# Performance work log

Measured on AMD Instinct MI355X. Metric: run time of the kernel, lower is better.

The kernel has to match this reference:

```python
import jax, jax.numpy as jnp
import numpy as np

D = 2048
N = 4096          # context length
H = N + 1         # Z columns (context + query)
LMBD = 0.9


def _decay_mask(h, n, lmbd, dtype=jnp.float32):
    # Closed form of the serial recurrence: M[r, c] = lmbd**(r-c) for c <= r < n, c < n; else 0.
    r = jnp.arange(h)
    diff = r[:, None] - r[None, :]
    valid = (diff >= 0) & (r[:, None] < n) & (r[None, :] < n)
    pow_ = jnp.asarray(lmbd, dtype) ** jnp.maximum(diff, 0).astype(dtype)
    return jnp.where(valid, pow_, jnp.zeros((), dtype))


def setup_inputs() -> dict:
    key = jax.random.key(0)
    kz, kp, kq = jax.random.split(key, 3)
    dim = 2 * D + 1
    Z = jax.random.normal(kz, (dim, H), dtype=jnp.float32)
    # params scaled like a typical init to keep the 5-GEMM chain numerically tame
    P = jax.random.normal(kp, (dim, dim), dtype=jnp.float32) * 0.02
    Q = jax.random.normal(kq, (dim, dim), dtype=jnp.float32) * 0.02
    return {"Z": Z, "P": P, "Q": Q}


def reference(Z, P, Q):
    h = Z.shape[1]
    M = _decay_mask(h, N, LMBD, Z.dtype)          # (h, h)
    left = (P @ Z) @ M                            # (2d+1, h)
    right = Z.T @ (Q @ Z)                         # (h, h)
    return Z + (left @ right) / N
```

## Files before the change

kernel.cpp:

```cpp
#include <hip/hip_runtime.h>


typedef __attribute__((ext_vector_type(8))) short short8;
typedef __attribute__((ext_vector_type(4))) float f32x4;
typedef __attribute__((ext_vector_type(4))) unsigned short u16x4;

#define NPAD 4352
#define NV   4097
#define NCTX 4096
#define NT   65
#define NT4  64

__device__ __forceinline__ float b2f(unsigned short u) {
  return __uint_as_float(((unsigned)u) << 16);
}
__device__ __forceinline__ unsigned short f2b(float f) {
  unsigned b = __float_as_uint(f);
  return (unsigned short)((b + 0x7FFFu + ((b >> 16) & 1u)) >> 16);
}
__device__ __forceinline__ void gload16(const void* g, void* l) {
  __builtin_amdgcn_global_load_lds(
      (const __attribute__((address_space(1))) unsigned int*)g,
      (__attribute__((address_space(3))) unsigned int*)l, 16, 0, 0);
}
__device__ __forceinline__ float wave_sum(float v) {
#pragma unroll
  for (int m = 1; m < 64; m <<= 1) v += __shfl_xor(v, m);
  return v;
}

__global__ __launch_bounds__(256) void cast_pad(const float* __restrict__ in,
                                                unsigned short* __restrict__ out) {
  int idx = blockIdx.x * 256 + threadIdx.x;
  int r = idx / 1088;
  int c4 = (idx - r * 1088) * 4;
  u16x4 o = {0, 0, 0, 0};
  if (r < NV) {
    const float* p = in + (size_t)r * NV + c4;
#pragma unroll
    for (int j = 0; j < 4; ++j) {
      float v = (c4 + j < NV) ? p[j] : 0.f;
      o[j] = f2b(v);
    }
  }
  *(u16x4*)&out[(size_t)r * NPAD + c4] = o;
}

__global__ __launch_bounds__(256) void transpose_cast(const float* __restrict__ in,
                                                      unsigned short* __restrict__ out) {
  __shared__ float tile[32][33];
  int x = threadIdx.x & 31;
  int y = threadIdx.x >> 5;
  int bx = blockIdx.x, by = blockIdx.y;
  int ic = bx * 32 + x;
#pragma unroll
  for (int j = 0; j < 4; ++j) {
    int ir = by * 32 + y + j * 8;
    float v = (ir < NV && ic < NV) ? in[(size_t)ir * NV + ic] : 0.f;
    tile[y + j * 8][x] = v;
  }
  __syncthreads();
  int orow = bx * 32;
  int ocol = by * 32 + x;
#pragma unroll
  for (int j = 0; j < 4; ++j) {
    out[(size_t)(orow + y + j * 8) * NPAD + ocol] = f2b(tile[x][y + j * 8]);
  }
}

__global__ __launch_bounds__(256) void decay_scan(const unsigned short* __restrict__ PZ,
                                                  unsigned short* __restrict__ L) {
  const int wid = (blockIdx.x << 2) | ((int)threadIdx.x >> 6);
  if (wid >= NV * 65) return;
  const int lane = threadIdx.x & 63;
  const int row = wid / 65;
  const int cj = wid - row * 65;
  const int c0 = cj * 64;

  const float l2l = -0.15200309344504995f;
  const float pl = exp2f((float)lane * l2l);
  const float plc = exp2f((float)(64 - lane) * l2l);

  const unsigned short* prow = PZ + (size_t)row * NPAD;
  float x[5];
#pragma unroll
  for (int d = 0; d < 5; ++d) {
    int c = c0 + d * 64 + lane;
    x[d] = (c < NCTX) ? b2f(prow[c]) : 0.f;
  }
  float s = x[0];
  const float pw[6] = {0.9f, 0.81f, 0.6561f, 0.43046721f,
                       0.18530201888518410f, 0.03433683820292512f};
#pragma unroll
  for (int i = 0; i < 6; ++i) {
    int tt = 1 << i;
    float o = __shfl_down(s, tt);
    s += (lane + tt < 64) ? pw[i] * o : 0.f;
  }
  const float cw[4] = {1.f, 1.1790184577738583e-3f, 1.3900845237714557e-6f,
                       1.6389541800e-9f};
  float carry = 0.f;
#pragma unroll
  for (int d = 1; d <= 4; ++d) {
    float v = x[d] * pl;
#pragma unroll
    for (int i = 0; i < 6; ++i) v += __shfl_xor(v, 1 << i);
    carry += cw[d - 1] * v;
  }
  float left = s + plc * carry;
  L[(size_t)row * NPAD + c0 + lane] = f2b(left);
}

template <int MODE>
__global__ __launch_bounds__(512, 2) void gemm256(
    const unsigned short* __restrict__ A0, const unsigned short* __restrict__ Bt0,
    unsigned short* __restrict__ C0,
    const unsigned short* __restrict__ A1, const unsigned short* __restrict__ Bt1,
    unsigned short* __restrict__ C1,
    float* __restrict__ Cf, const float* __restrict__ Zin) {
  __shared__ __align__(16) unsigned short Asm[2][256 * 64];
  __shared__ __align__(16) unsigned short Bsm[2][256 * 64];

  const int tid = threadIdx.x;
  const int lane = tid & 63;
  const int w = tid >> 6;
  const int wr = w >> 2, wc = w & 3;
  const int q = lane >> 4, r16 = lane & 15;

  const int NFULL = (MODE == 0) ? 512 : 256;
  const int cpx = NFULL >> 3;
  int orig = blockIdx.x;
  int wg = (orig & 7) * cpx + (orig >> 3);

  const unsigned short* Am;
  const unsigned short* Btm;
  unsigned short* Co;
  if (MODE == 0) {
    int batch = wg >> 8;
    Am = batch ? A1 : A0;
    Btm = batch ? Bt1 : Bt0;
    Co = batch ? C1 : C0;
    wg &= 255;
  } else {
    Am = A0; Btm = Bt0; Co = C0;
  }
  const int by = wg >> 4, bx = wg & 15;
  const int brow = by * 256, bcol = bx * 256;
  const int KE = (MODE == 2) ? NT4 : NT;

  auto stageA = [&](int ktile, int mq, int bb) {
#pragma unroll
    for (int it = 0; it < 2; ++it) {
      int sub = w * 16 + it * 8;
      int row0 = mq * 64 + sub + (sub & 64);
      int row = row0 + (lane >> 3);
      int win = (lane & 7) ^ (row & 7);
      gload16(Am + (size_t)(brow + row) * NPAD + ktile * 64 + win * 8,
              &Asm[bb][row0 * 64]);
    }
  };
  auto stageB = [&](int ktile, int nq, int bb) {
#pragma unroll
    for (int it = 0; it < 2; ++it) {
      int sub = w * 16 + it * 8;
      int row0 = ((sub >> 5) << 6) + nq * 32 + (sub & 31);
      int row = row0 + (lane >> 3);
      int win = (lane & 7) ^ (row & 7);
      gload16(Btm + (size_t)(bcol + row) * NPAD + ktile * 64 + win * 8,
              &Bsm[bb][row0 * 64]);
    }
  };

  short8 a[4][2], b0r[2][2], b1r[2][2];
  auto rdA = [&](int mq, int bb) {
#pragma unroll
    for (int m = 0; m < 4; ++m) {
      int row = wr * 128 + mq * 64 + m * 16 + r16;
#pragma unroll
      for (int kk = 0; kk < 2; ++kk) {
        int win = (q + kk * 4) ^ (r16 & 7);
        a[m][kk] = *(const short8*)&Asm[bb][row * 64 + win * 8];
      }
    }
  };
  auto rdB = [&](short8 (&b)[2][2], int nq, int bb) {
#pragma unroll
    for (int n = 0; n < 2; ++n) {
      int row = wc * 64 + nq * 32 + n * 16 + r16;
#pragma unroll
      for (int kk = 0; kk < 2; ++kk) {
        int win = (q + kk * 4) ^ (r16 & 7);
        b[n][kk] = *(const short8*)&Bsm[bb][row * 64 + win * 8];
      }
    }
  };

  f32x4 acc[8][4] = {};

  auto mma2 = [&](int mq) {
    __builtin_amdgcn_s_setprio(1);
#pragma unroll
    for (int kk = 0; kk < 2; ++kk)
#pragma unroll
      for (int m = 0; m < 4; ++m) {
#pragma unroll
        for (int n = 0; n < 2; ++n)
          acc[mq * 4 + m][n] = __builtin_amdgcn_mfma_f32_16x16x32_bf16(
              a[m][kk], b0r[n][kk], acc[mq * 4 + m][n], 0, 0, 0);
#pragma unroll
        for (int n = 0; n < 2; ++n)
          acc[mq * 4 + m][2 + n] = __builtin_amdgcn_mfma_f32_16x16x32_bf16(
              a[m][kk], b1r[n][kk], acc[mq * 4 + m][2 + n], 0, 0, 0);
      }
    __builtin_amdgcn_s_setprio(0);
  };

  stageA(0, 0, 0); stageB(0, 0, 0); stageA(0, 1, 0); stageB(0, 1, 0);
  stageA(1, 0, 1); stageB(1, 0, 1);
  asm volatile("s_waitcnt vmcnt(4)" ::: "memory");
  __builtin_amdgcn_s_barrier();

  for (int kt = 0; kt < KE; ++kt) {
    const int bb = kt & 1;
    rdA(0, bb);
    rdB(b0r, 0, bb);
    rdB(b1r, 1, bb);
    if (kt + 1 < KE) { stageA(kt + 1, 1, bb ^ 1); stageB(kt + 1, 1, bb ^ 1); }
    __builtin_amdgcn_s_barrier();
    mma2(0);
    __builtin_amdgcn_s_barrier();
    rdA(1, bb);
    if (kt + 2 < KE) { stageA(kt + 2, 0, bb); stageB(kt + 2, 0, bb); }
    if (kt < KE - 2) { asm volatile("s_waitcnt vmcnt(4)" ::: "memory"); }
    else             { asm volatile("s_waitcnt vmcnt(0)" ::: "memory"); }
    __builtin_amdgcn_s_barrier();
    mma2(1);
    __builtin_amdgcn_s_barrier();
  }

#pragma unroll
  for (int m = 0; m < 8; ++m) {
    const int row = brow + wr * 128 + m * 16 + q * 4;
#pragma unroll
    for (int n = 0; n < 4; ++n) {
      const int col = bcol + wc * 64 + n * 16 + r16;
#pragma unroll
      for (int v = 0; v < 4; ++v) {
        float val = acc[m][n][v];
        if (MODE == 2) {
          size_t o = (size_t)(row + v) * NV + col;
          Cf[o] = Zin[o] + val * (1.0f / 4096.0f);
        } else {
          Co[(size_t)(row + v) * NPAD + col] = f2b(val);
        }
      }
    }
  }
}

__global__ __launch_bounds__(256) void border1(
    const unsigned short* __restrict__ Pb, const unsigned short* __restrict__ Qb,
    const unsigned short* __restrict__ Zt,
    unsigned short* __restrict__ PZ, unsigned short* __restrict__ QZt) {
  const int wid = blockIdx.x * 4 + ((int)threadIdx.x >> 6);
  const int lane = threadIdx.x & 63;
  if (wid < 4096) {
    const int t = wid;
    const unsigned short* z = Zt + (size_t)t * NPAD;
    const unsigned short* p = Pb + (size_t)4096 * NPAD;
    const unsigned short* qq = Qb + (size_t)4096 * NPAD;
    float ap = 0.f, aq = 0.f;
    for (int k = lane * 8; k < 4104; k += 512) {
      short8 zv = *(const short8*)&z[k];
      short8 pv = *(const short8*)&p[k];
      short8 qv = *(const short8*)&qq[k];
#pragma unroll
      for (int j = 0; j < 8; ++j) {
        float zf = b2f((unsigned short)zv[j]);
        ap += zf * b2f((unsigned short)pv[j]);
        aq += zf * b2f((unsigned short)qv[j]);
      }
    }
    ap = wave_sum(ap);
    aq = wave_sum(aq);
    if (lane == 0) PZ[(size_t)4096 * NPAD + t] = f2b(ap);
    QZt[(size_t)t * NPAD + 4096 + lane] = (lane == 0) ? f2b(aq) : (unsigned short)0;
  } else {
    const int j = wid - 4096;
    if (j >= 4160) return;
    const unsigned short* qr = Qb + (size_t)j * NPAD;
    const unsigned short* zr = Zt + (size_t)4096 * NPAD;
    float a = 0.f;
    for (int k = lane * 8; k < 4104; k += 512) {
      short8 qv = *(const short8*)&qr[k];
      short8 zv = *(const short8*)&zr[k];
#pragma unroll
      for (int jj = 0; jj < 8; ++jj)
        a += b2f((unsigned short)qv[jj]) * b2f((unsigned short)zv[jj]);
    }
    a = wave_sum(a);
    if (lane == 0) QZt[(size_t)4096 * NPAD + j] = f2b(a);
  }
}

__global__ __launch_bounds__(256) void border2(const unsigned short* __restrict__ QZt,
                                               const unsigned short* __restrict__ Zt,
                                               unsigned short* __restrict__ RT) {
  const int t = blockIdx.x * 4 + ((int)threadIdx.x >> 6);
  const int lane = threadIdx.x & 63;
  const unsigned short* a = QZt + (size_t)4096 * NPAD;
  const unsigned short* z = Zt + (size_t)t * NPAD;
  float s = 0.f;
  for (int k = lane * 8; k < 4104; k += 512) {
    short8 av = *(const short8*)&a[k];
    short8 zv = *(const short8*)&z[k];
#pragma unroll
    for (int j = 0; j < 8; ++j)
      s += b2f((unsigned short)av[j]) * b2f((unsigned short)zv[j]);
  }
  s = wave_sum(s);
  if (lane == 0) RT[(size_t)4096 * NPAD + t] = f2b(s);
}

__global__ __launch_bounds__(256) void border3(const unsigned short* __restrict__ L,
                                               const unsigned short* __restrict__ RT,
                                               const float* __restrict__ Z,
                                               float* __restrict__ out) {
  const int wid = blockIdx.x * 4 + ((int)threadIdx.x >> 6);
  const int lane = threadIdx.x & 63;
  const unsigned short *lr, *rr;
  size_t o;
  if (wid < 4097) {
    lr = L + (size_t)4096 * NPAD;
    rr = RT + (size_t)wid * NPAD;
    o = (size_t)4096 * NV + wid;
  } else {
    const int r = wid - 4097;
    if (r >= 4096) return;
    lr = L + (size_t)r * NPAD;
    rr = RT + (size_t)4096 * NPAD;
    o = (size_t)r * NV + 4096;
  }
  float s = 0.f;
#pragma unroll 2
  for (int i = 0; i < 8; ++i) {
    int k = lane * 8 + i * 512;
    short8 lv = *(const short8*)&lr[k];
    short8 rv = *(const short8*)&rr[k];
#pragma unroll
    for (int j = 0; j < 8; ++j)
      s += b2f((unsigned short)lv[j]) * b2f((unsigned short)rv[j]);
  }
  s = wave_sum(s);
  if (lane == 0) out[o] = Z[o] + s * (1.0f / 4096.0f);
}

extern "C" void kernel_launch(void* const* d_in, const int* in_sizes, int n_in,
                              void* d_out, int out_size, void* d_ws, size_t ws_size,
                              hipStream_t stream) {
  (void)in_sizes; (void)n_in; (void)out_size; (void)ws_size;
  const float* Z = (const float*)d_in[0];
  const float* P = (const float*)d_in[1];
  const float* Q = (const float*)d_in[2];
  float* out = (float*)d_out;

  const size_t SZ = (size_t)NPAD * NPAD;
  unsigned short* b0 = (unsigned short*)d_ws;
  unsigned short* b1 = b0 + SZ;
  unsigned short* b2 = b1 + SZ;
  unsigned short* b3 = b2 + SZ;
  unsigned short* dox = (unsigned short*)d_out;

  dim3 blk(256), blk5(512);
  dim3 gt(136, 136);

  cast_pad<<<18496, blk, 0, stream>>>(P, b0);
  cast_pad<<<18496, blk, 0, stream>>>(Q, b3);
  transpose_cast<<<gt, blk, 0, stream>>>(Z, b1);
  gemm256<0><<<512, blk5, 0, stream>>>(b0, b1, b2, b1, b3, dox, nullptr, nullptr);
  border1<<<2064, blk, 0, stream>>>(b0, b3, b1, b2, dox);
  decay_scan<<<66577, blk, 0, stream>>>(b2, b0);
  gemm256<1><<<256, blk5, 0, stream>>>(dox, b1, b2, nullptr, nullptr, nullptr,
                                       nullptr, nullptr);
  border2<<<1024, blk, 0, stream>>>(dox, b1, b2);
  gemm256<2><<<256, blk5, 0, stream>>>(b0, b2, nullptr, nullptr, nullptr, nullptr,
                                       out, Z);
  border3<<<2049, blk, 0, stream>>>(b0, b2, Z, out);
}
```

Baseline: 666.8 us.

## Drop redundant GEMM barriers, widen decay scan per wave, merge cast kernels

Removes two of the four workgroup barriers per k-iteration in the main GEMM loop, on the reasoning that the remaining barriers already order LDS reuse between the staged buffers. The decay scan now has each wave handle four 64-column chunks and reuse the butterfly-reduced sums across overlapping carry windows, which cuts the number of waves and redundant shuffles. The two P/Q cast launches are merged into one grid. Risks: fewer barriers could expose LDS races. The scan no longer writes the padding columns at 4096 and above, so those columns of L keep whatever the buffer previously held (the cast of P) unless a later kernel handles them.

```diff
diff --git a/kernel.cpp b/kernel.cpp
--- a/kernel.cpp
+++ b/kernel.cpp
@@ -29,9 +29,15 @@
   return v;
 }
 
-__global__ __launch_bounds__(256) void cast_pad(const float* __restrict__ in,
-                                                unsigned short* __restrict__ out) {
-  int idx = blockIdx.x * 256 + threadIdx.x;
+__global__ __launch_bounds__(256) void cast_pad2(const float* __restrict__ inP,
+                                                 unsigned short* __restrict__ outP,
+                                                 const float* __restrict__ inQ,
+                                                 unsigned short* __restrict__ outQ) {
+  int bid = blockIdx.x;
+  const float* in = inP;
+  unsigned short* out = outP;
+  if (bid >= 18496) { bid -= 18496; in = inQ; out = outQ; }
+  int idx = bid * 256 + threadIdx.x;
   int r = idx / 1088;
   int c4 = (idx - r * 1088) * 4;
   u16x4 o = {0, 0, 0, 0};
@@ -71,44 +77,49 @@
 __global__ __launch_bounds__(256) void decay_scan(const unsigned short* __restrict__ PZ,
                                                   unsigned short* __restrict__ L) {
   const int wid = (blockIdx.x << 2) | ((int)threadIdx.x >> 6);
-  if (wid >= NV * 65) return;
+  if (wid >= NV * 16) return;
   const int lane = threadIdx.x & 63;
-  const int row = wid / 65;
-  const int cj = wid - row * 65;
-  const int c0 = cj * 64;
+  const int row = wid >> 4;
+  const int g = wid & 15;
+  const int c0 = g * 256;
 
   const float l2l = -0.15200309344504995f;
   const float pl = exp2f((float)lane * l2l);
   const float plc = exp2f((float)(64 - lane) * l2l);
 
   const unsigned short* prow = PZ + (size_t)row * NPAD;
-  float x[5];
-#pragma unroll
-  for (int d = 0; d < 5; ++d) {
+  float x[8];
+#pragma unroll
+  for (int d = 0; d < 8; ++d) {
     int c = c0 + d * 64 + lane;
     x[d] = (c < NCTX) ? b2f(prow[c]) : 0.f;
   }
-  float s = x[0];
+  float S[8];
+#pragma unroll
+  for (int d = 1; d < 8; ++d) {
+    float v = x[d] * pl;
+#pragma unroll
+    for (int i = 0; i < 6; ++i) v += __shfl_xor(v, 1 << i);
+    S[d] = v;
+  }
   const float pw[6] = {0.9f, 0.81f, 0.6561f, 0.43046721f,
                        0.18530201888518410f, 0.03433683820292512f};
-#pragma unroll
-  for (int i = 0; i < 6; ++i) {
-    int tt = 1 << i;
-    float o = __shfl_down(s, tt);
-    s += (lane + tt < 64) ? pw[i] * o : 0.f;
-  }
-  const float cw[4] = {1.f, 1.1790184577738583e-3f, 1.3900845237714557e-6f,
-                       1.6389541800e-9f};
-  float carry = 0.f;
-#pragma unroll
-  for (int d = 1; d <= 4; ++d) {
-    float v = x[d] * pl;
-#pragma unroll
-    for (int i = 0; i < 6; ++i) v += __shfl_xor(v, 1 << i);
-    carry += cw[d - 1] * v;
-  }
-  float left = s + plc * carry;
-  L[(size_t)row * NPAD + c0 + lane] = f2b(left);
+  const float cw1 = 1.1790184577738583e-3f;
+  const float cw2 = 1.3900845237714557e-6f;
+  const float cw3 = 1.6389541800e-9f;
+#pragma unroll
+  for (int j = 0; j < 4; ++j) {
+    float s = x[j];
+#pragma unroll
+    for (int i = 0; i < 6; ++i) {
+      int tt = 1 << i;
+      float o = __shfl_down(s, tt);
+      s += (lane + tt < 64) ? pw[i] * o : 0.f;
+    }
+    float carry = S[j + 1] + cw1 * S[j + 2] + cw2 * S[j + 3] + cw3 * S[j + 4];
+    float left = s + plc * carry;
+    L[(size_t)row * NPAD + c0 + j * 64 + lane] = f2b(left);
+  }
 }
 
 template <int MODE>
@@ -226,14 +237,12 @@
     rdB(b0r, 0, bb);
     rdB(b1r, 1, bb);
     if (kt + 1 < KE) { stageA(kt + 1, 1, bb ^ 1); stageB(kt + 1, 1, bb ^ 1); }
-    __builtin_amdgcn_s_barrier();
     mma2(0);
     __builtin_amdgcn_s_barrier();
     rdA(1, bb);
     if (kt + 2 < KE) { stageA(kt + 2, 0, bb); stageB(kt + 2, 0, bb); }
     if (kt < KE - 2) { asm volatile("s_waitcnt vmcnt(4)" ::: "memory"); }
     else             { asm volatile("s_waitcnt vmcnt(0)" ::: "memory"); }
-    __builtin_amdgcn_s_barrier();
     mma2(1);
     __builtin_amdgcn_s_barrier();
   }
@@ -374,12 +383,11 @@
   dim3 blk(256), blk5(512);
   dim3 gt(136, 136);
 
-  cast_pad<<<18496, blk, 0, stream>>>(P, b0);
-  cast_pad<<<18496, blk, 0, stream>>>(Q, b3);
+  cast_pad2<<<36992, blk, 0, stream>>>(P, b0, Q, b3);
   transpose_cast<<<gt, blk, 0, stream>>>(Z, b1);
   gemm256<0><<<512, blk5, 0, stream>>>(b0, b1, b2, b1, b3, dox, nullptr, nullptr);
   border1<<<2064, blk, 0, stream>>>(b0, b3, b1, b2, dox);
-  decay_scan<<<66577, blk, 0, stream>>>(b2, b0);
+  decay_scan<<<16388, blk, 0, stream>>>(b2, b0);
   gemm256<1><<<256, blk5, 0, stream>>>(dox, b1, b2, nullptr, nullptr, nullptr,
                                        nullptr, nullptr);
   border2<<<1024, blk, 0, stream>>>(dox, b1, b2);
```

New measurement: 606.0 us (median of 2 runs). -9.1%, faster.
